# Kernel tuning notes

Measured on AMD Instinct MI355X. Metric: run time of the kernel, lower is better.

The kernel has to match this reference:

```python
import jax, jax.numpy as jnp
import numpy as np

EPS = 1e-8  # torch F.cosine_similarity denominator clamp

def _row_cosine(a, b):
    # cosine similarity along last dim, rowwise: (N, D), (N, D) -> (N,)
    dot = jnp.sum(a * b, axis=-1)
    na = jnp.linalg.norm(a, axis=-1)
    nb = jnp.linalg.norm(b, axis=-1)
    return dot / jnp.maximum(na * nb, EPS)

def setup_inputs() -> dict:
    key = jax.random.key(0)
    k0, k1, k2, k3 = jax.random.split(key, 4)
    B, D, N = 4096, 256, 262144
    return {
        "anchor_emb": jax.random.normal(k0, (B, D), dtype=jnp.float32),
        "pos_emb": jax.random.normal(k1, (B, D), dtype=jnp.float32),
        "neg_emb": jax.random.normal(k2, (N, D), dtype=jnp.float32),
        "neg_batch_indices": jax.random.randint(k3, (N,), 0, B, dtype=jnp.int64),
    }

def reference(anchor_emb, pos_emb, neg_emb, neg_batch_indices):
    margin = 0.5
    B = anchor_emb.shape[0]
    # (B,) positive similarities
    pos_sim = _row_cosine(anchor_emb, pos_emb)
    # gather each negative's anchor: (N, D)
    anchor_g = anchor_emb[neg_batch_indices]
    neg_sims = _row_cosine(anchor_g, neg_emb)              # (N,)
    triplet = jnp.maximum(margin + neg_sims - pos_sim[neg_batch_indices], 0.0)  # (N,)
    # segment mean per batch item; empty segments contribute 0
    sums = jax.ops.segment_sum(triplet, neg_batch_indices, num_segments=B)
    counts = jax.ops.segment_sum(jnp.ones_like(triplet), neg_batch_indices, num_segments=B)
    means = jnp.where(counts > 0, sums / jnp.maximum(counts, 1.0), 0.0)
    return jnp.sum(means) / B
```

## Files before the change

### kernel.cpp

```cpp
#include <hip/hip_runtime.h>
#include <math.h>

#define EPS 1e-8f
#define MARGIN 0.5f
#define NEG_PER_WAVE 32
#define FIXSCALE 1048576.0f
#define MASK40 ((1ULL << 40) - 1)

typedef float    f4 __attribute__((ext_vector_type(4)));
typedef _Float16 h4 __attribute__((ext_vector_type(4)));

__device__ __forceinline__ float dot4(const f4 a, const f4 b) {
    return a.x * b.x + a.y * b.y + a.z * b.z + a.w * b.w;
}
__device__ __forceinline__ float dot4h(const h4 a, const f4 b) {
    return (float)a.x * b.x + (float)a.y * b.y + (float)a.z * b.z + (float)a.w * b.w;
}


__global__ void pos_h_kernel(const float* __restrict__ anchor,
                             const float* __restrict__ pos,
                             _Float16* __restrict__ a_h,
                             float* __restrict__ ps,
                             unsigned long long* __restrict__ acc,
                             int B) {
    const int tid  = blockIdx.x * blockDim.x + threadIdx.x;
    const int row  = tid >> 6;
    const int lane = threadIdx.x & 63;

    if (tid < 2 * B) ((unsigned int*)acc)[tid] = 0u;

    if (row >= B) return;

    const f4 a = *(reinterpret_cast<const f4*>(anchor + (size_t)row * 256) + lane);
    const f4 p = *(reinterpret_cast<const f4*>(pos    + (size_t)row * 256) + lane);

    float dot = dot4(a, p);
    float na  = dot4(a, a);
    float nb  = dot4(p, p);

    #pragma unroll
    for (int off = 32; off > 0; off >>= 1) {
        dot += __shfl_xor(dot, off);
        na  += __shfl_xor(na,  off);
        nb  += __shfl_xor(nb,  off);
    }
    const float sna   = sqrtf(na);
    const float scale = 1.0f / fmaxf(sna, 1e-20f);

    h4 ah;
    ah.x = (_Float16)(a.x * scale);
    ah.y = (_Float16)(a.y * scale);
    ah.z = (_Float16)(a.z * scale);
    ah.w = (_Float16)(a.w * scale);
    *(reinterpret_cast<h4*>(a_h + (size_t)row * 256) + lane) = ah;

    if (lane == 0)
        ps[row] = dot / fmaxf(sna * sqrtf(nb), EPS);
}

__global__ void __launch_bounds__(256) neg_h_kernel(
        const _Float16* __restrict__ a_h,
        const float* __restrict__ neg,
        const int*  __restrict__ idx,
        const float* __restrict__ ps,
        unsigned long long* __restrict__ acc,
        int N) {
    __shared__ float ssim[4][NEG_PER_WAVE];

    const int lane  = threadIdx.x & 63;
    const int wid   = threadIdx.x >> 6;
    const int group = lane >> 4;
    const int glane = lane & 15;
    const long long base =
        ((long long)blockIdx.x * (blockDim.x >> 6) + wid) * NEG_PER_WAVE;

    int b_all = 0;
    {
        const long long in = base + lane;
        if (lane < NEG_PER_WAVE && in < N) b_all = idx[in];
    }

    if (base < N) {
        #pragma unroll 4
        for (int it = 0; it < NEG_PER_WAVE; it += 4) {
            const long long n = base + it + group;
            const bool valid = (n < N);
            const long long ns = valid ? n : (long long)0;
            const int b = __shfl(b_all, it + group);

            const f4* nr = reinterpret_cast<const f4*>(neg + (size_t)ns * 256);
            const h4* ar = reinterpret_cast<const h4*>(a_h + (size_t)b * 256);

            const f4 v0 = nr[ 0 + glane];
            const f4 v1 = nr[16 + glane];
            const f4 v2 = nr[32 + glane];
            const f4 v3 = nr[48 + glane];
            const h4 a0 = ar[ 0 + glane], a1 = ar[16 + glane],
                     a2 = ar[32 + glane], a3 = ar[48 + glane];

            float d = dot4h(a0, v0) + dot4h(a1, v1) + dot4h(a2, v2) + dot4h(a3, v3);
            float q = dot4(v0, v0) + dot4(v1, v1) + dot4(v2, v2) + dot4(v3, v3);

            #pragma unroll
            for (int off = 8; off > 0; off >>= 1) {
                d += __shfl_xor(d, off);
                q += __shfl_xor(q, off);
            }
            if (glane == 0)
                ssim[wid][it + group] = d * rsqrtf(fmaxf(q, 1e-30f));
        }
    }

    if (lane < NEG_PER_WAVE && base + lane < N) {
        const float t = fmaxf(MARGIN + ssim[wid][lane] - ps[b_all], 0.0f);
        const unsigned long long pk =
            (unsigned long long)(t * FIXSCALE + 0.5f) + (1ULL << 40);
        atomicAdd(&acc[b_all], pk);
    }
}

__global__ void __launch_bounds__(1024) finalize_packed_kernel(
        const unsigned long long* __restrict__ acc,
        float* __restrict__ out, int B) {
    float local = 0.0f;
    for (int i = threadIdx.x; i < B; i += blockDim.x) {
        const unsigned long long v = acc[i];
        const float c = (float)(v >> 40);
        const float s = (float)(v & MASK40) * (1.0f / FIXSCALE);
        local += (c > 0.0f) ? (s / c) : 0.0f;
    }
    #pragma unroll
    for (int off = 32; off > 0; off >>= 1)
        local += __shfl_xor(local, off);

    __shared__ float ws[16];
    const int wid = threadIdx.x >> 6;
    if ((threadIdx.x & 63) == 0) ws[wid] = local;
    __syncthreads();
    if (threadIdx.x == 0) {
        float tot = 0.0f;
        const int nw = blockDim.x >> 6;
        for (int w = 0; w < nw; ++w) tot += ws[w];
        out[0] = tot / (float)B;
    }
}


__global__ void pos_sim_kernel(const float* __restrict__ anchor,
                               const float* __restrict__ pos,
                               float2* __restrict__ pn,
                               float* __restrict__ sums,
                               float* __restrict__ counts,
                               int B) {
    const int tid  = blockIdx.x * blockDim.x + threadIdx.x;
    const int wave = tid >> 6;
    const int lane = threadIdx.x & 63;
    if (tid < B) sums[tid] = 0.0f;
    else if (tid < 2 * B) counts[tid - B] = 0.0f;
    if (wave >= B) return;
    const f4 a = *(reinterpret_cast<const f4*>(anchor + (size_t)wave * 256) + lane);
    const f4 p = *(reinterpret_cast<const f4*>(pos    + (size_t)wave * 256) + lane);
    float dot = dot4(a, p), na = dot4(a, a), nb = dot4(p, p);
    #pragma unroll
    for (int off = 32; off > 0; off >>= 1) {
        dot += __shfl_xor(dot, off);
        na  += __shfl_xor(na,  off);
        nb  += __shfl_xor(nb,  off);
    }
    if (lane == 0) {
        float sna = sqrtf(na);
        float2 r; r.x = dot / fmaxf(sna * sqrtf(nb), EPS); r.y = sna;
        pn[wave] = r;
    }
}

__global__ void __launch_bounds__(256) neg_kernel(
        const float* __restrict__ anchor,
        const float* __restrict__ neg,
        const int*  __restrict__ idx,
        const float2* __restrict__ pn,
        float* __restrict__ sums,
        float* __restrict__ counts,
        int N) {
    const int lane  = threadIdx.x & 63;
    const int wid   = threadIdx.x >> 6;
    const int group = lane >> 4;
    const int glane = lane & 15;
    const long long base =
        ((long long)blockIdx.x * (blockDim.x >> 6) + wid) * NEG_PER_WAVE;
    if (base >= N) return;
    for (int it = 0; it < NEG_PER_WAVE; it += 4) {
        const long long n = base + it + group;
        if (n >= N) continue;
        const int b = idx[n];
        const f4* ar = reinterpret_cast<const f4*>(anchor + (size_t)b * 256);
        const f4* nr = reinterpret_cast<const f4*>(neg + (size_t)n * 256);
        float d = 0.0f, q = 0.0f;
        #pragma unroll
        for (int c = 0; c < 4; ++c) {
            const f4 a = ar[c * 16 + glane];
            const f4 v = nr[c * 16 + glane];
            d += dot4(a, v); q += dot4(v, v);
        }
        #pragma unroll
        for (int off = 8; off > 0; off >>= 1) {
            d += __shfl_xor(d, off);
            q += __shfl_xor(q, off);
        }
        if (glane == 0) {
            const float2 p = pn[b];
            float t = fmaxf(MARGIN + d / fmaxf(p.y * sqrtf(q), EPS) - p.x, 0.0f);
            atomicAdd(&sums[b], t);
            atomicAdd(&counts[b], 1.0f);
        }
    }
}

__global__ void __launch_bounds__(1024) finalize_kernel(
        const float* __restrict__ sums,
        const float* __restrict__ counts,
        float* __restrict__ out, int B) {
    float local = 0.0f;
    for (int i = threadIdx.x; i < B; i += blockDim.x) {
        float c = counts[i];
        local += (c > 0.0f) ? (sums[i] / c) : 0.0f;
    }
    #pragma unroll
    for (int off = 32; off > 0; off >>= 1)
        local += __shfl_xor(local, off);

    __shared__ float ws[16];
    const int wid = threadIdx.x >> 6;
    if ((threadIdx.x & 63) == 0) ws[wid] = local;
    __syncthreads();
    if (threadIdx.x == 0) {
        float tot = 0.0f;
        const int nw = blockDim.x >> 6;
        for (int w = 0; w < nw; ++w) tot += ws[w];
        out[0] = tot / (float)B;
    }
}

extern "C" void kernel_launch(void* const* d_in, const int* in_sizes, int n_in,
                              void* d_out, int out_size, void* d_ws, size_t ws_size,
                              hipStream_t stream) {
    const float* anchor = (const float*)d_in[0];
    const float* pos    = (const float*)d_in[1];
    const float* neg    = (const float*)d_in[2];
    const int*   idx    = (const int*)d_in[3];

    const int D = 256;
    int B = in_sizes[0] / D;
    int N = in_sizes[3];

    const size_t need_h = (size_t)B * 256 * sizeof(_Float16)
                        + (size_t)B * sizeof(float)
                        + (size_t)B * sizeof(unsigned long long);

    const int threads = 256;
    const int negs_per_block = (threads / 64) * NEG_PER_WAVE;
    const int nblocks = (N + negs_per_block - 1) / negs_per_block;

    if (ws_size >= need_h) {
        _Float16*           a_h = (_Float16*)d_ws;
        float*              ps  = (float*)(a_h + (size_t)B * 256);
        unsigned long long* acc = (unsigned long long*)(ps + B);

        pos_h_kernel<<<(B + 3) / 4, threads, 0, stream>>>(anchor, pos, a_h, ps,
                                                          acc, B);
        neg_h_kernel<<<nblocks, threads, 0, stream>>>(a_h, neg, idx, ps,
                                                      acc, N);
        finalize_packed_kernel<<<1, 1024, 0, stream>>>(acc, (float*)d_out, B);
    } else {
        float2* pn     = (float2*)d_ws;
        float*  sums   = (float*)(pn + B);
        float*  counts = sums + B;

        pos_sim_kernel<<<(B + 3) / 4, threads, 0, stream>>>(anchor, pos, pn,
                                                            sums, counts, B);
        neg_kernel<<<nblocks, threads, 0, stream>>>(anchor, neg, idx, pn,
                                                    sums, counts, N);
        finalize_kernel<<<1, 1024, 0, stream>>>(sums, counts, (float*)d_out, B);
    }
}
```

Before: 61.79 us.

## Counting-sort negatives by anchor index and segment-reduce atomics per wave

Adds a histogram, prefix scan and scatter pass that sorts negative indices by their anchor. The negative kernel then walks the sorted order, so anchor rows get reused and adjacent lanes sharing an anchor are combined before a single atomic. This is meant to cut atomic contention and scattered anchor gathers. In exchange it adds four extra launches plus a memset, an N-sized sorted buffer, and randomly permuted reads of negative rows, which were contiguous before. The old fp32 fallback path is removed, and unroll drops from 4 to 2.

```diff
diff --git a/kernel.cpp b/kernel.cpp
--- a/kernel.cpp
+++ b/kernel.cpp
@@ -15,6 +15,200 @@
 }
 __device__ __forceinline__ float dot4h(const h4 a, const f4 b) {
     return (float)a.x * b.x + (float)a.y * b.y + (float)a.z * b.z + (float)a.w * b.w;
+}
+
+
+__global__ void pos_hist_kernel(const float* __restrict__ anchor,
+                                const float* __restrict__ pos,
+                                const int*  __restrict__ idx,
+                                _Float16* __restrict__ a_h,
+                                float* __restrict__ ps,
+                                unsigned long long* __restrict__ acc,
+                                unsigned* __restrict__ cnt,
+                                int B, int N) {
+    const int tid  = blockIdx.x * blockDim.x + threadIdx.x;
+    const int row  = tid >> 6;
+    const int lane = threadIdx.x & 63;
+    const int tot  = gridDim.x * blockDim.x;
+
+    if (tid < 2 * B) ((unsigned int*)acc)[tid] = 0u;
+
+    for (long long i = tid; i < N; i += tot)
+        atomicAdd(&cnt[idx[i]], 1u);
+
+    if (row >= B) return;
+
+    const f4 a = *(reinterpret_cast<const f4*>(anchor + (size_t)row * 256) + lane);
+    const f4 p = *(reinterpret_cast<const f4*>(pos    + (size_t)row * 256) + lane);
+
+    float dot = dot4(a, p);
+    float na  = dot4(a, a);
+    float nb  = dot4(p, p);
+
+    #pragma unroll
+    for (int off = 32; off > 0; off >>= 1) {
+        dot += __shfl_xor(dot, off);
+        na  += __shfl_xor(na,  off);
+        nb  += __shfl_xor(nb,  off);
+    }
+    const float sna   = sqrtf(na);
+    const float scale = 1.0f / fmaxf(sna, 1e-20f);
+
+    h4 ah;
+    ah.x = (_Float16)(a.x * scale);
+    ah.y = (_Float16)(a.y * scale);
+    ah.z = (_Float16)(a.z * scale);
+    ah.w = (_Float16)(a.w * scale);
+    *(reinterpret_cast<h4*>(a_h + (size_t)row * 256) + lane) = ah;
+
+    if (lane == 0)
+        ps[row] = dot / fmaxf(sna * sqrtf(nb), EPS);
+}
+
+__global__ void __launch_bounds__(1024) scan_kernel(
+        const unsigned* __restrict__ cnt,
+        unsigned* __restrict__ off, int B) {
+    __shared__ unsigned tsum[1024];
+    const int t = threadIdx.x;
+    unsigned c[4];
+    unsigned s = 0;
+    #pragma unroll
+    for (int j = 0; j < 4; ++j) {
+        const int i = t * 4 + j;
+        c[j] = (i < B) ? cnt[i] : 0u;
+        s += c[j];
+    }
+    tsum[t] = s;
+    __syncthreads();
+    for (int o = 1; o < 1024; o <<= 1) {
+        const unsigned v = (t >= o) ? tsum[t - o] : 0u;
+        __syncthreads();
+        tsum[t] += v;
+        __syncthreads();
+    }
+    unsigned pre = (t > 0) ? tsum[t - 1] : 0u;
+    #pragma unroll
+    for (int j = 0; j < 4; ++j) {
+        const int i = t * 4 + j;
+        if (i < B) off[i] = pre;
+        pre += c[j];
+    }
+}
+
+__global__ void scatter_kernel(const int* __restrict__ idx,
+                               unsigned* __restrict__ off,
+                               unsigned long long* __restrict__ sorted,
+                               int N) {
+    const int i = blockIdx.x * blockDim.x + threadIdx.x;
+    if (i < N) {
+        const int b = idx[i];
+        const unsigned p = atomicAdd(&off[b], 1u);
+        sorted[p] = ((unsigned long long)(unsigned)b << 32) | (unsigned)i;
+    }
+}
+
+__global__ void __launch_bounds__(256) neg_h_sorted(
+        const _Float16* __restrict__ a_h,
+        const float* __restrict__ neg,
+        const unsigned long long* __restrict__ sorted,
+        const float* __restrict__ ps,
+        unsigned long long* __restrict__ acc,
+        int N) {
+    __shared__ float ssim[4][NEG_PER_WAVE];
+
+    const int lane  = threadIdx.x & 63;
+    const int wid   = threadIdx.x >> 6;
+    const int group = lane >> 4;
+    const int glane = lane & 15;
+    const long long base =
+        ((long long)blockIdx.x * (blockDim.x >> 6) + wid) * NEG_PER_WAVE;
+
+    int b_all = -1, n_all = 0;
+    if (lane < NEG_PER_WAVE) {
+        const long long ii = base + lane;
+        if (ii < N) {
+            const unsigned long long e = sorted[ii];
+            b_all = (int)(e >> 32);
+            n_all = (int)(e & 0xffffffffu);
+        }
+    }
+
+    if (base < N) {
+        #pragma unroll 2
+        for (int it = 0; it < NEG_PER_WAVE; it += 4) {
+            const bool valid = (base + it + group) < N;
+            const int b = __shfl(b_all, it + group);
+            const int n = __shfl(n_all, it + group);
+            const int nn = valid ? n : 0;
+            const int bb = valid ? b : 0;
+
+            const f4* nr = reinterpret_cast<const f4*>(neg + (size_t)nn * 256);
+            const h4* ar = reinterpret_cast<const h4*>(a_h + (size_t)bb * 256);
+
+            const f4 v0 = nr[ 0 + glane];
+            const f4 v1 = nr[16 + glane];
+            const f4 v2 = nr[32 + glane];
+            const f4 v3 = nr[48 + glane];
+            const h4 a0 = ar[ 0 + glane], a1 = ar[16 + glane],
+                     a2 = ar[32 + glane], a3 = ar[48 + glane];
+
+            float d = dot4h(a0, v0) + dot4h(a1, v1) + dot4h(a2, v2) + dot4h(a3, v3);
+            float q = dot4(v0, v0) + dot4(v1, v1) + dot4(v2, v2) + dot4(v3, v3);
+
+            #pragma unroll
+            for (int off = 8; off > 0; off >>= 1) {
+                d += __shfl_xor(d, off);
+                q += __shfl_xor(q, off);
+            }
+            if (glane == 0 && valid)
+                ssim[wid][it + group] = d * rsqrtf(fmaxf(q, 1e-30f));
+        }
+    }
+
+    unsigned long long pk = 0;
+    int bseg = -1;
+    if (lane < NEG_PER_WAVE && base + lane < N) {
+        bseg = b_all;
+        const float t = fmaxf(MARGIN + ssim[wid][lane] - ps[bseg], 0.0f);
+        pk = (unsigned long long)(t * FIXSCALE + 0.5f) + (1ULL << 40);
+    }
+    #pragma unroll
+    for (int o = 1; o < NEG_PER_WAVE; o <<= 1) {
+        const int nb = __shfl_down(bseg, o);
+        const unsigned long long nv = __shfl_down(pk, o);
+        if (lane + o < 64 && nb == bseg) pk += nv;
+    }
+    if (bseg >= 0) {
+        const int pb = __shfl_up(bseg, 1);
+        if (lane == 0 || pb != bseg)
+            atomicAdd(&acc[bseg], pk);
+    }
+}
+
+__global__ void __launch_bounds__(1024) finalize_packed_kernel(
+        const unsigned long long* __restrict__ acc,
+        float* __restrict__ out, int B) {
+    float local = 0.0f;
+    for (int i = threadIdx.x; i < B; i += blockDim.x) {
+        const unsigned long long v = acc[i];
+        const float c = (float)(v >> 40);
+        const float s = (float)(v & MASK40) * (1.0f / FIXSCALE);
+        local += (c > 0.0f) ? (s / c) : 0.0f;
+    }
+    #pragma unroll
+    for (int off = 32; off > 0; off >>= 1)
+        local += __shfl_xor(local, off);
+
+    __shared__ float ws[16];
+    const int wid = threadIdx.x >> 6;
+    if ((threadIdx.x & 63) == 0) ws[wid] = local;
+    __syncthreads();
+    if (threadIdx.x == 0) {
+        float tot = 0.0f;
+        const int nw = blockDim.x >> 6;
+        for (int w = 0; w < nw; ++w) tot += ws[w];
+        out[0] = tot / (float)B;
+    }
 }
 
 
@@ -29,16 +223,12 @@
     const int lane = threadIdx.x & 63;
 
     if (tid < 2 * B) ((unsigned int*)acc)[tid] = 0u;
-
     if (row >= B) return;
 
     const f4 a = *(reinterpret_cast<const f4*>(anchor + (size_t)row * 256) + lane);
     const f4 p = *(reinterpret_cast<const f4*>(pos    + (size_t)row * 256) + lane);
 
-    float dot = dot4(a, p);
-    float na  = dot4(a, a);
-    float nb  = dot4(p, p);
-
+    float dot = dot4(a, p), na = dot4(a, a), nb = dot4(p, p);
     #pragma unroll
     for (int off = 32; off > 0; off >>= 1) {
         dot += __shfl_xor(dot, off);
@@ -47,16 +237,11 @@
     }
     const float sna   = sqrtf(na);
     const float scale = 1.0f / fmaxf(sna, 1e-20f);
-
     h4 ah;
-    ah.x = (_Float16)(a.x * scale);
-    ah.y = (_Float16)(a.y * scale);
-    ah.z = (_Float16)(a.z * scale);
-    ah.w = (_Float16)(a.w * scale);
+    ah.x = (_Float16)(a.x * scale); ah.y = (_Float16)(a.y * scale);
+    ah.z = (_Float16)(a.z * scale); ah.w = (_Float16)(a.w * scale);
     *(reinterpret_cast<h4*>(a_h + (size_t)row * 256) + lane) = ah;
-
-    if (lane == 0)
-        ps[row] = dot / fmaxf(sna * sqrtf(nb), EPS);
+    if (lane == 0) ps[row] = dot / fmaxf(sna * sqrtf(nb), EPS);
 }
 
 __global__ void __launch_bounds__(256) neg_h_kernel(
@@ -67,7 +252,6 @@
         unsigned long long* __restrict__ acc,
         int N) {
     __shared__ float ssim[4][NEG_PER_WAVE];
-
     const int lane  = threadIdx.x & 63;
     const int wid   = threadIdx.x >> 6;
     const int group = lane >> 4;
@@ -80,9 +264,8 @@
         const long long in = base + lane;
         if (lane < NEG_PER_WAVE && in < N) b_all = idx[in];
     }
-
     if (base < N) {
-        #pragma unroll 4
+        #pragma unroll 2
         for (int it = 0; it < NEG_PER_WAVE; it += 4) {
             const long long n = base + it + group;
             const bool valid = (n < N);
@@ -91,154 +274,27 @@
 
             const f4* nr = reinterpret_cast<const f4*>(neg + (size_t)ns * 256);
             const h4* ar = reinterpret_cast<const h4*>(a_h + (size_t)b * 256);
-
-            const f4 v0 = nr[ 0 + glane];
-            const f4 v1 = nr[16 + glane];
-            const f4 v2 = nr[32 + glane];
-            const f4 v3 = nr[48 + glane];
+            const f4 v0 = nr[ 0 + glane], v1 = nr[16 + glane],
+                     v2 = nr[32 + glane], v3 = nr[48 + glane];
             const h4 a0 = ar[ 0 + glane], a1 = ar[16 + glane],
                      a2 = ar[32 + glane], a3 = ar[48 + glane];
 
             float d = dot4h(a0, v0) + dot4h(a1, v1) + dot4h(a2, v2) + dot4h(a3, v3);
             float q = dot4(v0, v0) + dot4(v1, v1) + dot4(v2, v2) + dot4(v3, v3);
-
             #pragma unroll
             for (int off = 8; off > 0; off >>= 1) {
                 d += __shfl_xor(d, off);
                 q += __shfl_xor(q, off);
             }
-            if (glane == 0)
+            if (glane == 0 && valid)
                 ssim[wid][it + group] = d * rsqrtf(fmaxf(q, 1e-30f));
         }
     }
-
     if (lane < NEG_PER_WAVE && base + lane < N) {
         const float t = fmaxf(MARGIN + ssim[wid][lane] - ps[b_all], 0.0f);
         const unsigned long long pk =
             (unsigned long long)(t * FIXSCALE + 0.5f) + (1ULL << 40);
         atomicAdd(&acc[b_all], pk);
-    }
-}
-
-__global__ void __launch_bounds__(1024) finalize_packed_kernel(
-        const unsigned long long* __restrict__ acc,
-        float* __restrict__ out, int B) {
-    float local = 0.0f;
-    for (int i = threadIdx.x; i < B; i += blockDim.x) {
-        const unsigned long long v = acc[i];
-        const float c = (float)(v >> 40);
-        const float s = (float)(v & MASK40) * (1.0f / FIXSCALE);
-        local += (c > 0.0f) ? (s / c) : 0.0f;
-    }
-    #pragma unroll
-    for (int off = 32; off > 0; off >>= 1)
-        local += __shfl_xor(local, off);
-
-    __shared__ float ws[16];
-    const int wid = threadIdx.x >> 6;
-    if ((threadIdx.x & 63) == 0) ws[wid] = local;
-    __syncthreads();
-    if (threadIdx.x == 0) {
-        float tot = 0.0f;
-        const int nw = blockDim.x >> 6;
-        for (int w = 0; w < nw; ++w) tot += ws[w];
-        out[0] = tot / (float)B;
-    }
-}
-
-
-__global__ void pos_sim_kernel(const float* __restrict__ anchor,
-                               const float* __restrict__ pos,
-                               float2* __restrict__ pn,
-                               float* __restrict__ sums,
-                               float* __restrict__ counts,
-                               int B) {
-    const int tid  = blockIdx.x * blockDim.x + threadIdx.x;
-    const int wave = tid >> 6;
-    const int lane = threadIdx.x & 63;
-    if (tid < B) sums[tid] = 0.0f;
-    else if (tid < 2 * B) counts[tid - B] = 0.0f;
-    if (wave >= B) return;
-    const f4 a = *(reinterpret_cast<const f4*>(anchor + (size_t)wave * 256) + lane);
-    const f4 p = *(reinterpret_cast<const f4*>(pos    + (size_t)wave * 256) + lane);
-    float dot = dot4(a, p), na = dot4(a, a), nb = dot4(p, p);
-    #pragma unroll
-    for (int off = 32; off > 0; off >>= 1) {
-        dot += __shfl_xor(dot, off);
-        na  += __shfl_xor(na,  off);
-        nb  += __shfl_xor(nb,  off);
-    }
-    if (lane == 0) {
-        float sna = sqrtf(na);
-        float2 r; r.x = dot / fmaxf(sna * sqrtf(nb), EPS); r.y = sna;
-        pn[wave] = r;
-    }
-}
-
-__global__ void __launch_bounds__(256) neg_kernel(
-        const float* __restrict__ anchor,
-        const float* __restrict__ neg,
-        const int*  __restrict__ idx,
-        const float2* __restrict__ pn,
-        float* __restrict__ sums,
-        float* __restrict__ counts,
-        int N) {
-    const int lane  = threadIdx.x & 63;
-    const int wid   = threadIdx.x >> 6;
-    const int group = lane >> 4;
-    const int glane = lane & 15;
-    const long long base =
-        ((long long)blockIdx.x * (blockDim.x >> 6) + wid) * NEG_PER_WAVE;
-    if (base >= N) return;
-    for (int it = 0; it < NEG_PER_WAVE; it += 4) {
-        const long long n = base + it + group;
-        if (n >= N) continue;
-        const int b = idx[n];
-        const f4* ar = reinterpret_cast<const f4*>(anchor + (size_t)b * 256);
-        const f4* nr = reinterpret_cast<const f4*>(neg + (size_t)n * 256);
-        float d = 0.0f, q = 0.0f;
-        #pragma unroll
-        for (int c = 0; c < 4; ++c) {
-            const f4 a = ar[c * 16 + glane];
-            const f4 v = nr[c * 16 + glane];
-            d += dot4(a, v); q += dot4(v, v);
-        }
-        #pragma unroll
-        for (int off = 8; off > 0; off >>= 1) {
-            d += __shfl_xor(d, off);
-            q += __shfl_xor(q, off);
-        }
-        if (glane == 0) {
-            const float2 p = pn[b];
-            float t = fmaxf(MARGIN + d / fmaxf(p.y * sqrtf(q), EPS) - p.x, 0.0f);
-            atomicAdd(&sums[b], t);
-            atomicAdd(&counts[b], 1.0f);
-        }
-    }
-}
-
-__global__ void __launch_bounds__(1024) finalize_kernel(
-        const float* __restrict__ sums,
-        const float* __restrict__ counts,
-        float* __restrict__ out, int B) {
-    float local = 0.0f;
-    for (int i = threadIdx.x; i < B; i += blockDim.x) {
-        float c = counts[i];
-        local += (c > 0.0f) ? (sums[i] / c) : 0.0f;
-    }
-    #pragma unroll
-    for (int off = 32; off > 0; off >>= 1)
-        local += __shfl_xor(local, off);
-
-    __shared__ float ws[16];
-    const int wid = threadIdx.x >> 6;
-    if ((threadIdx.x & 63) == 0) ws[wid] = local;
-    __syncthreads();
-    if (threadIdx.x == 0) {
-        float tot = 0.0f;
-        const int nw = blockDim.x >> 6;
-        for (int w = 0; w < nw; ++w) tot += ws[w];
-        out[0] = tot / (float)B;
     }
 }
 
@@ -254,33 +310,37 @@
     int B = in_sizes[0] / D;
     int N = in_sizes[3];
 
-    const size_t need_h = (size_t)B * 256 * sizeof(_Float16)
-                        + (size_t)B * sizeof(float)
-                        + (size_t)B * sizeof(unsigned long long);
-
     const int threads = 256;
     const int negs_per_block = (threads / 64) * NEG_PER_WAVE;
     const int nblocks = (N + negs_per_block - 1) / negs_per_block;
 
-    if (ws_size >= need_h) {
-        _Float16*           a_h = (_Float16*)d_ws;
-        float*              ps  = (float*)(a_h + (size_t)B * 256);
-        unsigned long long* acc = (unsigned long long*)(ps + B);
-
+    size_t o = 0;
+    _Float16*           a_h    = (_Float16*)d_ws;            o += (size_t)B * 256 * sizeof(_Float16);
+    float*              ps     = (float*)((char*)d_ws + o);  o += (size_t)B * sizeof(float);
+    unsigned long long* acc    = (unsigned long long*)((char*)d_ws + o); o += (size_t)B * sizeof(unsigned long long);
+    unsigned*           cnt    = (unsigned*)((char*)d_ws + o); o += (size_t)B * sizeof(unsigned);
+    unsigned*           offb   = (unsigned*)((char*)d_ws + o); o += (size_t)B * sizeof(unsigned);
+    unsigned long long* sorted = (unsigned long long*)((char*)d_ws + o); o += (size_t)N * sizeof(unsigned long long);
+    const size_t need_sorted = o;
+    const size_t need_plain  = (size_t)B * 256 * sizeof(_Float16)
+                             + (size_t)B * sizeof(float)
+                             + (size_t)B * sizeof(unsigned long long);
+
+    if (ws_size >= need_sorted && B <= 4096) {
+        hipMemsetAsync(cnt, 0, (size_t)B * sizeof(unsigned), stream);
+        pos_hist_kernel<<<(B + 3) / 4, threads, 0, stream>>>(
+            anchor, pos, idx, a_h, ps, acc, cnt, B, N);
+        scan_kernel<<<1, 1024, 0, stream>>>(cnt, offb, B);
+        scatter_kernel<<<(N + threads - 1) / threads, threads, 0, stream>>>(
+            idx, offb, sorted, N);
+        neg_h_sorted<<<nblocks, threads, 0, stream>>>(a_h, neg, sorted, ps,
+                                                      acc, N);
+        finalize_packed_kernel<<<1, 1024, 0, stream>>>(acc, (float*)d_out, B);
+    } else if (ws_size >= need_plain) {
         pos_h_kernel<<<(B + 3) / 4, threads, 0, stream>>>(anchor, pos, a_h, ps,
                                                           acc, B);
         neg_h_kernel<<<nblocks, threads, 0, stream>>>(a_h, neg, idx, ps,
                                                       acc, N);
         finalize_packed_kernel<<<1, 1024, 0, stream>>>(acc, (float*)d_out, B);
-    } else {
-        float2* pn     = (float2*)d_ws;
-        float*  sums   = (float*)(pn + B);
-        float*  counts = sums + B;
-
-        pos_sim_kernel<<<(B + 3) / 4, threads, 0, stream>>>(anchor, pos, pn,
-                                                            sums, counts, B);
-        neg_kernel<<<nblocks, threads, 0, stream>>>(anchor, neg, idx, pn,
-                                                    sums, counts, N);
-        finalize_kernel<<<1, 1024, 0, stream>>>(sums, counts, (float*)d_out, B);
-    }
-}
+    }
+}
```

After: 100.4 us. 1.63x slower.
